# Kernel tuning notes

Measured on AMD Instinct MI355X. Metric: run time of the kernel, lower is better.

The kernel has to match this reference:

```python
import jax, jax.numpy as jnp
import numpy as np

N_GOAL, N_OBS, N_TASK = 16384, 65536, 8192
E1, E2 = 1048576, 1048576
B = 256            # graphs in batch
F, S = 128, 64     # dim_features, dim_state


def setup_inputs() -> dict:
    key = jax.random.key(0)
    ks = jax.random.split(key, 16)
    inp = {
        "x_goal": jax.random.normal(ks[0], (N_GOAL, F), jnp.float32),
        "x_obs": jax.random.normal(ks[1], (N_OBS, F), jnp.float32),
        "x_task": jax.random.normal(ks[2], (N_TASK, S), jnp.float32),
        "ei_go_src": jax.random.randint(ks[3], (E1,), 0, N_GOAL),
        "ei_go_dst": jax.random.randint(ks[4], (E1,), 0, N_OBS),
        "ei_ot_src": jax.random.randint(ks[5], (E2,), 0, N_OBS),
        "ei_ot_dst": jax.random.randint(ks[6], (E2,), 0, N_TASK),
        # contiguous graph assignment: 32 task nodes per graph
        "task_batch": jnp.arange(N_TASK) // (N_TASK // B),
        # GinStandardMLP (state_gin): Lin(F,S)-ReLU-Lin(S,S)-ReLU
        "W1": jax.random.normal(ks[7], (F, S), jnp.float32) * 0.05,
        "b1": jnp.zeros((S,), jnp.float32),
        "W2": jax.random.normal(ks[8], (S, S), jnp.float32) * 0.05,
        "b2": jnp.zeros((S,), jnp.float32),
        # GinUnactivatedMLP (action_gin): Lin(S,S)-ReLU-Lin(S,1)
        "W3": jax.random.normal(ks[9], (S, S), jnp.float32) * 0.05,
        "b3": jnp.zeros((S,), jnp.float32),
        "W4": jax.random.normal(ks[10], (S, 1), jnp.float32) * 0.05,
        "b4": jnp.zeros((1,), jnp.float32),
        # critic head: Lin(2,8)-ReLU-Lin(8,1)
        "Wc1": jax.random.normal(ks[11], (2, 8), jnp.float32) * 0.5,
        "bc1": jnp.zeros((8,), jnp.float32),
        "Wc2": jax.random.normal(ks[12], (8, 1), jnp.float32) * 0.5,
        "bc2": jnp.zeros((1,), jnp.float32),
    }
    return inp


def reference(x_goal, x_obs, x_task,
              ei_go_src, ei_go_dst, ei_ot_src, ei_ot_dst, task_batch,
              W1, b1, W2, b2, W3, b3, W4, b4, Wc1, bc1, Wc2, bc2):
    # --- state_gin: GINConv((goal, obs)), eps=0 ---
    agg1 = jax.ops.segment_sum(x_goal[ei_go_src], ei_go_dst, num_segments=N_OBS)
    h = x_obs + agg1                              # (1+eps)*x_dst + sum_j x_src
    h = jax.nn.relu(h @ W1 + b1)
    x1 = jax.nn.relu(h @ W2 + b2)                 # [N_OBS, S]

    # --- action_gin: GINConv((obs, task)), eps=0 ---
    agg2 = jax.ops.segment_sum(x1[ei_ot_src], ei_ot_dst, num_segments=N_TASK)
    g = x_task + agg2
    g = jax.nn.relu(g @ W3 + b3)
    x2 = g @ W4 + b4                              # [N_TASK, 1]

    # --- critic path: global max / mean pool over task nodes per graph ---
    max_pool = jax.ops.segment_max(x2, task_batch, num_segments=B)   # [B, 1]
    cnt = jax.ops.segment_sum(jnp.ones((N_TASK, 1), x2.dtype), task_batch, num_segments=B)
    mean_pool = jax.ops.segment_sum(x2, task_batch, num_segments=B) / cnt  # [B, 1]

    pooled = jnp.concatenate([max_pool.max(axis=1, keepdims=True),
                              mean_pool.mean(axis=1, keepdims=True)], axis=1)  # [B, 2]
    out = jax.nn.relu(pooled @ Wc1 + bc1) @ Wc2 + bc2                 # [B, 1]
    return out.squeeze(-1)                                            # [B]
```

## Files before the change

### kernel.cpp

```cpp
#include <hip/hip_runtime.h>
#include <hip/hip_bf16.h>


#define CAP1 2816
#define CAP2 5120
#define GEMM_BLKS 640

__global__ __launch_bounds__(256) void prep(
    const float* __restrict__ x_goal, const float* __restrict__ x_obs,
    const float* __restrict__ W, float* __restrict__ xg1,
    float* __restrict__ obs,
    const int* __restrict__ go_src, const int* __restrict__ go_dst,
    const int* __restrict__ ot_src, const int* __restrict__ ot_dst,
    int* __restrict__ gcur1, int* __restrict__ gcur2,
    int* __restrict__ pairs1, int* __restrict__ pairs2, int nblk1, int nblk2,
    const float* __restrict__ W2, const float* __restrict__ W3,
    float* __restrict__ w2t_g, float* __restrict__ w3t_g)
{
    __shared__ float smem[8192];
    const int tid = threadIdx.x;

    if (blockIdx.x < GEMM_BLKS) {
        const float* X;
        float* O;
        int row0;
        if (blockIdx.x < 128) { X = x_goal; O = xg1; row0 = blockIdx.x * 128; }
        else                  { X = x_obs;  O = obs; row0 = (blockIdx.x - 128) * 128; }
        const int c0 = (tid & 7) * 8;
        const int trow = tid >> 3;
        const int r0 = trow * 4;
        const int swz = trow & 7;
        const int w = tid >> 6;
        const int lane = tid & 63;
        const int srow = w * 32 + (lane >> 3);
        const int skbx = lane & 7;

        float acc[4][8];
        #pragma unroll
        for (int i = 0; i < 4; ++i)
            #pragma unroll
            for (int j = 0; j < 8; ++j) acc[i][j] = 0.f;

        float* bufA = smem;
        float* bufB = smem + 4096;

        auto stage = [&](float* buf, int k0) {
            #pragma unroll
            for (int m = 0; m < 4; ++m) {
                int row = srow + m * 8;
                int kg = skbx ^ ((row >> 2) & 7);
                const float* gp = X + (size_t)(row0 + row) * 128 + k0 + kg * 4;
                __builtin_amdgcn_global_load_lds(
                    (const __attribute__((address_space(1))) unsigned int*)gp,
                    (__attribute__((address_space(3))) unsigned int*)
                        (buf + (w * 4 + m) * 256),
                    16, 0, 0);
            }
        };

        stage(bufA, 0);
        __syncthreads();

        float* cur = bufA;
        float* nxt = bufB;
        for (int kc = 0; kc < 4; ++kc) {
            const int k0 = kc * 32;
            if (kc < 3) stage(nxt, k0 + 32);
            #pragma unroll 2
            for (int kb = 0; kb < 8; ++kb) {
                float4 xv[4];
                #pragma unroll
                for (int i = 0; i < 4; ++i)
                    xv[i] = *(const float4*)(cur + (r0 + i) * 32 + ((kb ^ swz) << 2));
                #pragma unroll
                for (int kk = 0; kk < 4; ++kk) {
                    const float* wp = W + (size_t)(k0 + kb * 4 + kk) * 64 + c0;
                    float4 w0 = *(const float4*)(wp);
                    float4 w1 = *(const float4*)(wp + 4);
                    #pragma unroll
                    for (int i = 0; i < 4; ++i) {
                        float xk = (kk == 0) ? xv[i].x : (kk == 1) ? xv[i].y
                                 : (kk == 2) ? xv[i].z : xv[i].w;
                        acc[i][0] = fmaf(xk, w0.x, acc[i][0]);
                        acc[i][1] = fmaf(xk, w0.y, acc[i][1]);
                        acc[i][2] = fmaf(xk, w0.z, acc[i][2]);
                        acc[i][3] = fmaf(xk, w0.w, acc[i][3]);
                        acc[i][4] = fmaf(xk, w1.x, acc[i][4]);
                        acc[i][5] = fmaf(xk, w1.y, acc[i][5]);
                        acc[i][6] = fmaf(xk, w1.z, acc[i][6]);
                        acc[i][7] = fmaf(xk, w1.w, acc[i][7]);
                    }
                }
            }
            __syncthreads();
            float* t = cur; cur = nxt; nxt = t;
        }
        #pragma unroll
        for (int i = 0; i < 4; ++i) {
            float4 o0; o0.x = acc[i][0]; o0.y = acc[i][1]; o0.z = acc[i][2]; o0.w = acc[i][3];
            float4 o1; o1.x = acc[i][4]; o1.y = acc[i][5]; o1.z = acc[i][6]; o1.w = acc[i][7];
            float* p = O + (size_t)(row0 + r0 + i) * 64 + c0;
            *(float4*)p = o0;
            *(float4*)(p + 4) = o1;
        }
    } else if (blockIdx.x < GEMM_BLKS + nblk1 + nblk2) {
        int* hist = (int*)smem;
        int* cur  = (int*)smem + 512;
        const int blk2 = blockIdx.x - GEMM_BLKS;
        const bool s1 = blk2 < nblk1;
        const int* src = s1 ? go_src : ot_src;
        const int* dst = s1 ? go_dst : ot_dst;
        int* gcur  = s1 ? gcur1 : gcur2;
        int* pairs = s1 ? pairs1 : pairs2;
        const int bsh  = s1 ? 7 : 5;
        const int rowm = s1 ? 127 : 31;
        const int nb   = s1 ? 512 : 256;
        const int cap  = s1 ? CAP1 : CAP2;
        const int blk  = s1 ? blk2 : blk2 - nblk1;

        for (int i = tid; i < nb; i += 256) hist[i] = 0;
        __syncthreads();
        const int base = blk * 4096;
        const int4* d4 = (const int4*)(dst + base);
        const int4* s4 = (const int4*)(src + base);
        int4 dv[4];
        #pragma unroll
        for (int k = 0; k < 4; ++k) {
            dv[k] = d4[k * 256 + tid];
            atomicAdd(&hist[dv[k].x >> bsh], 1);
            atomicAdd(&hist[dv[k].y >> bsh], 1);
            atomicAdd(&hist[dv[k].z >> bsh], 1);
            atomicAdd(&hist[dv[k].w >> bsh], 1);
        }
        __syncthreads();
        for (int i = tid; i < nb; i += 256)
            cur[i] = atomicAdd(&gcur[i], hist[i]);
        __syncthreads();
        #pragma unroll
        for (int k = 0; k < 4; ++k) {
            int4 sv = s4[k * 256 + tid];
            int d, s, b, p;
            d = dv[k].x; s = sv.x; b = d >> bsh; p = atomicAdd(&cur[b], 1);
            if (p < cap) pairs[(size_t)b * cap + p] = ((d & rowm) << 17) | s;
            d = dv[k].y; s = sv.y; b = d >> bsh; p = atomicAdd(&cur[b], 1);
            if (p < cap) pairs[(size_t)b * cap + p] = ((d & rowm) << 17) | s;
            d = dv[k].z; s = sv.z; b = d >> bsh; p = atomicAdd(&cur[b], 1);
            if (p < cap) pairs[(size_t)b * cap + p] = ((d & rowm) << 17) | s;
            d = dv[k].w; s = sv.w; b = d >> bsh; p = atomicAdd(&cur[b], 1);
            if (p < cap) pairs[(size_t)b * cap + p] = ((d & rowm) << 17) | s;
        }
    } else {
        for (int i = tid; i < 4352; i += 256) {
            int c = i / 68, k = i % 68;
            float v2 = (k < 64) ? W2[k * 64 + c] : 0.f;
            float v3 = (k < 64) ? W3[k * 64 + c] : 0.f;
            w2t_g[i] = v2;
            w3t_g[i] = v3;
        }
    }
}

__global__ __launch_bounds__(1024) void gather_mlp_obs(
    const int* __restrict__ pairs, const int* __restrict__ cnt,
    const float* __restrict__ xg1, const float* __restrict__ obs,
    const float* __restrict__ b1, const float* __restrict__ w2t_g,
    const float* __restrict__ b2, float* __restrict__ x1)
{
    constexpr int ROWS = 128;
    __shared__ __align__(16) int ssrc[CAP1];
    __shared__ int offs[ROWS + 1];
    __shared__ int rcnt[ROWS];
    __shared__ __align__(16) float W2t[64 * 68];
    __shared__ __align__(16) float hb[16 * 64];
    const int tid = threadIdx.x;
    const int b = blockIdx.x;

    #pragma unroll
    for (int i = tid; i < 4352; i += 1024) W2t[i] = w2t_g[i];
    if (tid < ROWS) rcnt[tid] = 0;
    __syncthreads();
    int n = cnt[b];
    if (n > CAP1) n = CAP1;
    const int* bp = pairs + (size_t)b * CAP1;

    int e0 = -1, e1 = -1, e2 = -1;
    {
        int i = tid;
        if (i < n) {
            e0 = bp[i]; atomicAdd(&rcnt[e0 >> 17], 1); i += 1024;
            if (i < n) {
                e1 = bp[i]; atomicAdd(&rcnt[e1 >> 17], 1); i += 1024;
                if (i < n) { e2 = bp[i]; atomicAdd(&rcnt[e2 >> 17], 1); }
            }
        }
    }
    __syncthreads();
    if (tid < 64) {
        int v0 = rcnt[2 * tid], v1 = rcnt[2 * tid + 1];
        int s = v0 + v1;
        #pragma unroll
        for (int d = 1; d < 64; d <<= 1) {
            int t = __shfl_up(s, d);
            if (tid >= d) s += t;
        }
        int ex = s - v0 - v1;
        offs[2 * tid] = ex;
        offs[2 * tid + 1] = ex + v0;
        rcnt[2 * tid] = ex;
        rcnt[2 * tid + 1] = ex + v0;
        if (tid == 63) offs[ROWS] = s;
    }
    __syncthreads();
    if (e0 >= 0) { int p = atomicAdd(&rcnt[e0 >> 17], 1); ssrc[p] = e0 & 0x1FFFF; }
    if (e1 >= 0) { int p = atomicAdd(&rcnt[e1 >> 17], 1); ssrc[p] = e1 & 0x1FFFF; }
    if (e2 >= 0) { int p = atomicAdd(&rcnt[e2 >> 17], 1); ssrc[p] = e2 & 0x1FFFF; }
    __syncthreads();
    const int wv = tid >> 6;
    const int lane = tid & 63;
    const float bb1 = b1[lane];
    const float bb2 = b2[lane];
    float* hp = hb + wv * 64;
    const float4* h4 = (const float4*)hp;
    const float4* wrow = (const float4*)(W2t + lane * 68);
    for (int r = wv; r < ROWS; r += 16) {
        int beg = offs[r], end = offs[r + 1];
        size_t gi = (((size_t)b * ROWS) + r) * 64 + lane;
        float base = obs[gi];
        float a0 = 0.f, a1 = 0.f, a2 = 0.f, a3 = 0.f;
        float a4 = 0.f, a5 = 0.f, a6 = 0.f, a7 = 0.f;
        int e = beg;
        for (; e < end && (e & 3); ++e)
            a0 += xg1[(size_t)ssrc[e] * 64 + lane];
        for (; e + 8 <= end; e += 8) {
            int4 s0 = *(const int4*)(ssrc + e);
            int4 s1 = *(const int4*)(ssrc + e + 4);
            a0 += xg1[(size_t)s0.x * 64 + lane];
            a1 += xg1[(size_t)s0.y * 64 + lane];
            a2 += xg1[(size_t)s0.z * 64 + lane];
            a3 += xg1[(size_t)s0.w * 64 + lane];
            a4 += xg1[(size_t)s1.x * 64 + lane];
            a5 += xg1[(size_t)s1.y * 64 + lane];
            a6 += xg1[(size_t)s1.z * 64 + lane];
            a7 += xg1[(size_t)s1.w * 64 + lane];
        }
        for (; e + 4 <= end; e += 4) {
            int4 s0 = *(const int4*)(ssrc + e);
            a0 += xg1[(size_t)s0.x * 64 + lane];
            a1 += xg1[(size_t)s0.y * 64 + lane];
            a2 += xg1[(size_t)s0.z * 64 + lane];
            a3 += xg1[(size_t)s0.w * 64 + lane];
        }
        for (; e < end; ++e)
            a0 += xg1[(size_t)ssrc[e] * 64 + lane];
        float acc = ((a0 + a1) + (a2 + a3)) + ((a4 + a5) + (a6 + a7)) + base;
        hp[lane] = fmaxf(acc + bb1, 0.f);
        float a = bb2;
        #pragma unroll 8
        for (int kc = 0; kc < 16; ++kc) {
            float4 hv = h4[kc];
            float4 wv4 = wrow[kc];
            a = fmaf(hv.x, wv4.x, a);
            a = fmaf(hv.y, wv4.y, a);
            a = fmaf(hv.z, wv4.z, a);
            a = fmaf(hv.w, wv4.w, a);
        }
        x1[gi] = fmaxf(a, 0.f);
    }
}

__global__ __launch_bounds__(1024) void gather_mlp_task_pool(
    const int* __restrict__ pairs, const int* __restrict__ cnt,
    const float* __restrict__ x1, const float* __restrict__ x_task,
    const float* __restrict__ w3t_g, const float* __restrict__ b3,
    const float* __restrict__ W4, const float* __restrict__ b4,
    const float* __restrict__ Wc1, const float* __restrict__ bc1,
    const float* __restrict__ Wc2, const float* __restrict__ bc2,
    float* __restrict__ out)
{
    constexpr int ROWS = 32;
    __shared__ __align__(16) int ssrc[CAP2];
    __shared__ int offs[ROWS + 1];
    __shared__ int rcnt[ROWS];
    __shared__ __align__(16) float W3t[64 * 68];
    __shared__ __align__(16) float hb[16 * 64];
    __shared__ float xrow[ROWS];
    const int tid = threadIdx.x;
    const int b = blockIdx.x;

    #pragma unroll
    for (int i = tid; i < 4352; i += 1024) W3t[i] = w3t_g[i];
    if (tid < ROWS) rcnt[tid] = 0;
    __syncthreads();
    int n = cnt[b];
    if (n > CAP2) n = CAP2;
    const int* bp = pairs + (size_t)b * CAP2;

    int e0 = -1, e1 = -1, e2 = -1, e3 = -1, e4 = -1;
    {
        int i = tid;
        if (i < n) { e0 = bp[i]; atomicAdd(&rcnt[e0 >> 17], 1); i += 1024;
        if (i < n) { e1 = bp[i]; atomicAdd(&rcnt[e1 >> 17], 1); i += 1024;
        if (i < n) { e2 = bp[i]; atomicAdd(&rcnt[e2 >> 17], 1); i += 1024;
        if (i < n) { e3 = bp[i]; atomicAdd(&rcnt[e3 >> 17], 1); i += 1024;
        if (i < n) { e4 = bp[i]; atomicAdd(&rcnt[e4 >> 17], 1); } } } } }
    }
    __syncthreads();
    if (tid < 32) {
        int v = rcnt[tid];
        int s = v;
        #pragma unroll
        for (int d = 1; d < 32; d <<= 1) {
            int t = __shfl_up(s, d);
            if (tid >= d) s += t;
        }
        int ex = s - v;
        offs[tid] = ex;
        rcnt[tid] = ex;
        if (tid == 31) offs[ROWS] = s;
    }
    __syncthreads();
    if (e0 >= 0) { int p = atomicAdd(&rcnt[e0 >> 17], 1); ssrc[p] = e0 & 0x1FFFF; }
    if (e1 >= 0) { int p = atomicAdd(&rcnt[e1 >> 17], 1); ssrc[p] = e1 & 0x1FFFF; }
    if (e2 >= 0) { int p = atomicAdd(&rcnt[e2 >> 17], 1); ssrc[p] = e2 & 0x1FFFF; }
    if (e3 >= 0) { int p = atomicAdd(&rcnt[e3 >> 17], 1); ssrc[p] = e3 & 0x1FFFF; }
    if (e4 >= 0) { int p = atomicAdd(&rcnt[e4 >> 17], 1); ssrc[p] = e4 & 0x1FFFF; }
    __syncthreads();

    const int wv = tid >> 6;
    const int lane = tid & 63;
    const float bb3 = b3[lane];
    const float w4l = W4[lane];
    const float b4c = b4[0];
    float* hp = hb + wv * 64;
    const float4* h4 = (const float4*)hp;
    const float4* wrow = (const float4*)(W3t + lane * 68);
    #pragma unroll
    for (int half = 0; half < 2; ++half) {
        const int r = wv + half * 16;
        const int row = b * ROWS + r;
        int beg = offs[r], end = offs[r + 1];
        float base = x_task[(size_t)row * 64 + lane];
        float a0 = 0.f, a1 = 0.f, a2 = 0.f, a3 = 0.f;
        float a4 = 0.f, a5 = 0.f, a6 = 0.f, a7 = 0.f;
        int e = beg;
        for (; e < end && (e & 3); ++e)
            a0 += x1[(size_t)ssrc[e] * 64 + lane];
        for (; e + 8 <= end; e += 8) {
            int4 s0 = *(const int4*)(ssrc + e);
            int4 s1 = *(const int4*)(ssrc + e + 4);
            a0 += x1[(size_t)s0.x * 64 + lane];
            a1 += x1[(size_t)s0.y * 64 + lane];
            a2 += x1[(size_t)s0.z * 64 + lane];
            a3 += x1[(size_t)s0.w * 64 + lane];
            a4 += x1[(size_t)s1.x * 64 + lane];
            a5 += x1[(size_t)s1.y * 64 + lane];
            a6 += x1[(size_t)s1.z * 64 + lane];
            a7 += x1[(size_t)s1.w * 64 + lane];
        }
        for (; e + 4 <= end; e += 4) {
            int4 s0 = *(const int4*)(ssrc + e);
            a0 += x1[(size_t)s0.x * 64 + lane];
            a1 += x1[(size_t)s0.y * 64 + lane];
            a2 += x1[(size_t)s0.z * 64 + lane];
            a3 += x1[(size_t)s0.w * 64 + lane];
        }
        for (; e < end; ++e)
            a0 += x1[(size_t)ssrc[e] * 64 + lane];
        float t = ((a0 + a1) + (a2 + a3)) + ((a4 + a5) + (a6 + a7)) + base;
        hp[lane] = t;
        float a = bb3;
        #pragma unroll 8
        for (int kc = 0; kc < 16; ++kc) {
            float4 hv = h4[kc];
            float4 wv4 = wrow[kc];
            a = fmaf(hv.x, wv4.x, a);
            a = fmaf(hv.y, wv4.y, a);
            a = fmaf(hv.z, wv4.z, a);
            a = fmaf(hv.w, wv4.w, a);
        }
        float p = fmaxf(a, 0.f) * w4l;
        p += __shfl_xor(p, 1);
        p += __shfl_xor(p, 2);
        p += __shfl_xor(p, 4);
        p += __shfl_xor(p, 8);
        p += __shfl_xor(p, 16);
        p += __shfl_xor(p, 32);
        if (lane == 0) xrow[r] = p + b4c;
    }
    __syncthreads();
    if (tid == 0) {
        float mx = -1e30f, sm = 0.f;
        #pragma unroll
        for (int i = 0; i < ROWS; ++i) {
            float v = xrow[i];
            mx = fmaxf(mx, v);
            sm += v;
        }
        float mn = sm * (1.f / 32.f);
        float o = bc2[0];
        #pragma unroll
        for (int j = 0; j < 8; ++j) {
            float t = fmaxf(mx * Wc1[j] + mn * Wc1[8 + j] + bc1[j], 0.f);
            o = fmaf(t, Wc2[j], o);
        }
        out[b] = o;
    }
}

extern "C" void kernel_launch(void* const* d_in, const int* in_sizes, int n_in,
                              void* d_out, int out_size, void* d_ws, size_t ws_size,
                              hipStream_t stream)
{
    const float* x_goal = (const float*)d_in[0];
    const float* x_obs  = (const float*)d_in[1];
    const float* x_task = (const float*)d_in[2];
    const int* go_src = (const int*)d_in[3];
    const int* go_dst = (const int*)d_in[4];
    const int* ot_src = (const int*)d_in[5];
    const int* ot_dst = (const int*)d_in[6];
    const float* W1  = (const float*)d_in[8];
    const float* b1  = (const float*)d_in[9];
    const float* W2  = (const float*)d_in[10];
    const float* b2  = (const float*)d_in[11];
    const float* W3  = (const float*)d_in[12];
    const float* b3  = (const float*)d_in[13];
    const float* W4  = (const float*)d_in[14];
    const float* b4  = (const float*)d_in[15];
    const float* Wc1 = (const float*)d_in[16];
    const float* bc1 = (const float*)d_in[17];
    const float* Wc2 = (const float*)d_in[18];
    const float* bc2 = (const float*)d_in[19];
    float* out = (float*)d_out;

    const int N_OBS = 65536, N_GOAL = 16384;
    const int E1 = in_sizes[3], E2 = in_sizes[5];
    const int NB1 = 512, NB2 = 256;

    char* w = (char*)d_ws;
    float* obs    = (float*)w;  w += (size_t)N_OBS * 64 * 4;
    float* x1     = (float*)w;  w += (size_t)N_OBS * 64 * 4;
    float* xg1    = (float*)w;  w += (size_t)N_GOAL * 64 * 4;
    int*   pairs1 = (int*)w;    w += (size_t)NB1 * CAP1 * 4;
    int*   pairs2 = (int*)w;    w += (size_t)NB2 * CAP2 * 4;
    int*   gcur1  = (int*)w;    w += NB1 * 4;
    int*   gcur2  = (int*)w;    w += NB2 * 4;
    float* w2t_g  = (float*)w;  w += 64 * 68 * 4;
    float* w3t_g  = (float*)w;  w += 64 * 68 * 4;

    hipMemsetAsync(gcur1, 0, (NB1 + NB2) * 4, stream);

    const int nblk1 = E1 / 4096;
    const int nblk2 = E2 / 4096;
    prep<<<GEMM_BLKS + nblk1 + nblk2 + 1, 256, 0, stream>>>(
        x_goal, x_obs, W1, xg1, obs,
        go_src, go_dst, ot_src, ot_dst, gcur1, gcur2, pairs1, pairs2,
        nblk1, nblk2, W2, W3, w2t_g, w3t_g);
    gather_mlp_obs<<<NB1, 1024, 0, stream>>>(pairs1, gcur1, xg1, obs, b1, w2t_g, b2, x1);
    gather_mlp_task_pool<<<NB2, 1024, 0, stream>>>(pairs2, gcur2, x1, x_task,
                                                   w3t_g, b3, W4, b4,
                                                   Wc1, bc1, Wc2, bc2, out);
}
```

Measured before the change: 230.7 us.

## Fuse obs and task gather kernels with a global completion counter

Merges the two gather+MLP kernels into one launch. The first 512 blocks handle obs rows and increment a device-scope done counter. The remaining 256 blocks build their task-edge CSR in shared memory first, then spin until all obs blocks finish before gathering x1. This is meant to remove a kernel launch boundary and overlap the task-side edge bucketing with the obs phase. It risks deadlock if the spinning blocks take up CUs before the obs blocks are scheduled; that relies on in-order block dispatch. Spinning also wastes occupancy.

```diff
diff --git a/kernel.cpp b/kernel.cpp
--- a/kernel.cpp
+++ b/kernel.cpp
@@ -5,6 +5,8 @@
 #define CAP1 2816
 #define CAP2 5120
 #define GEMM_BLKS 640
+#define NB1 512
+#define NB2 256
 
 __global__ __launch_bounds__(256) void prep(
     const float* __restrict__ x_goal, const float* __restrict__ x_obs,
@@ -160,250 +162,262 @@
     }
 }
 
-__global__ __launch_bounds__(1024) void gather_mlp_obs(
-    const int* __restrict__ pairs, const int* __restrict__ cnt,
+__global__ __launch_bounds__(1024) void gather_fused(
+    const int* __restrict__ pairs1, const int* __restrict__ gcur1,
+    const int* __restrict__ pairs2, const int* __restrict__ gcur2,
     const float* __restrict__ xg1, const float* __restrict__ obs,
     const float* __restrict__ b1, const float* __restrict__ w2t_g,
-    const float* __restrict__ b2, float* __restrict__ x1)
-{
-    constexpr int ROWS = 128;
-    __shared__ __align__(16) int ssrc[CAP1];
-    __shared__ int offs[ROWS + 1];
-    __shared__ int rcnt[ROWS];
-    __shared__ __align__(16) float W2t[64 * 68];
-    __shared__ __align__(16) float hb[16 * 64];
-    const int tid = threadIdx.x;
-    const int b = blockIdx.x;
-
-    #pragma unroll
-    for (int i = tid; i < 4352; i += 1024) W2t[i] = w2t_g[i];
-    if (tid < ROWS) rcnt[tid] = 0;
-    __syncthreads();
-    int n = cnt[b];
-    if (n > CAP1) n = CAP1;
-    const int* bp = pairs + (size_t)b * CAP1;
-
-    int e0 = -1, e1 = -1, e2 = -1;
-    {
-        int i = tid;
-        if (i < n) {
-            e0 = bp[i]; atomicAdd(&rcnt[e0 >> 17], 1); i += 1024;
-            if (i < n) {
-                e1 = bp[i]; atomicAdd(&rcnt[e1 >> 17], 1); i += 1024;
-                if (i < n) { e2 = bp[i]; atomicAdd(&rcnt[e2 >> 17], 1); }
-            }
-        }
-    }
-    __syncthreads();
-    if (tid < 64) {
-        int v0 = rcnt[2 * tid], v1 = rcnt[2 * tid + 1];
-        int s = v0 + v1;
-        #pragma unroll
-        for (int d = 1; d < 64; d <<= 1) {
-            int t = __shfl_up(s, d);
-            if (tid >= d) s += t;
-        }
-        int ex = s - v0 - v1;
-        offs[2 * tid] = ex;
-        offs[2 * tid + 1] = ex + v0;
-        rcnt[2 * tid] = ex;
-        rcnt[2 * tid + 1] = ex + v0;
-        if (tid == 63) offs[ROWS] = s;
-    }
-    __syncthreads();
-    if (e0 >= 0) { int p = atomicAdd(&rcnt[e0 >> 17], 1); ssrc[p] = e0 & 0x1FFFF; }
-    if (e1 >= 0) { int p = atomicAdd(&rcnt[e1 >> 17], 1); ssrc[p] = e1 & 0x1FFFF; }
-    if (e2 >= 0) { int p = atomicAdd(&rcnt[e2 >> 17], 1); ssrc[p] = e2 & 0x1FFFF; }
-    __syncthreads();
-    const int wv = tid >> 6;
-    const int lane = tid & 63;
-    const float bb1 = b1[lane];
-    const float bb2 = b2[lane];
-    float* hp = hb + wv * 64;
-    const float4* h4 = (const float4*)hp;
-    const float4* wrow = (const float4*)(W2t + lane * 68);
-    for (int r = wv; r < ROWS; r += 16) {
-        int beg = offs[r], end = offs[r + 1];
-        size_t gi = (((size_t)b * ROWS) + r) * 64 + lane;
-        float base = obs[gi];
-        float a0 = 0.f, a1 = 0.f, a2 = 0.f, a3 = 0.f;
-        float a4 = 0.f, a5 = 0.f, a6 = 0.f, a7 = 0.f;
-        int e = beg;
-        for (; e < end && (e & 3); ++e)
-            a0 += xg1[(size_t)ssrc[e] * 64 + lane];
-        for (; e + 8 <= end; e += 8) {
-            int4 s0 = *(const int4*)(ssrc + e);
-            int4 s1 = *(const int4*)(ssrc + e + 4);
-            a0 += xg1[(size_t)s0.x * 64 + lane];
-            a1 += xg1[(size_t)s0.y * 64 + lane];
-            a2 += xg1[(size_t)s0.z * 64 + lane];
-            a3 += xg1[(size_t)s0.w * 64 + lane];
-            a4 += xg1[(size_t)s1.x * 64 + lane];
-            a5 += xg1[(size_t)s1.y * 64 + lane];
-            a6 += xg1[(size_t)s1.z * 64 + lane];
-            a7 += xg1[(size_t)s1.w * 64 + lane];
-        }
-        for (; e + 4 <= end; e += 4) {
-            int4 s0 = *(const int4*)(ssrc + e);
-            a0 += xg1[(size_t)s0.x * 64 + lane];
-            a1 += xg1[(size_t)s0.y * 64 + lane];
-            a2 += xg1[(size_t)s0.z * 64 + lane];
-            a3 += xg1[(size_t)s0.w * 64 + lane];
-        }
-        for (; e < end; ++e)
-            a0 += xg1[(size_t)ssrc[e] * 64 + lane];
-        float acc = ((a0 + a1) + (a2 + a3)) + ((a4 + a5) + (a6 + a7)) + base;
-        hp[lane] = fmaxf(acc + bb1, 0.f);
-        float a = bb2;
-        #pragma unroll 8
-        for (int kc = 0; kc < 16; ++kc) {
-            float4 hv = h4[kc];
-            float4 wv4 = wrow[kc];
-            a = fmaf(hv.x, wv4.x, a);
-            a = fmaf(hv.y, wv4.y, a);
-            a = fmaf(hv.z, wv4.z, a);
-            a = fmaf(hv.w, wv4.w, a);
-        }
-        x1[gi] = fmaxf(a, 0.f);
-    }
-}
-
-__global__ __launch_bounds__(1024) void gather_mlp_task_pool(
-    const int* __restrict__ pairs, const int* __restrict__ cnt,
-    const float* __restrict__ x1, const float* __restrict__ x_task,
+    const float* __restrict__ b2, float* __restrict__ x1,
+    const float* __restrict__ x_task,
     const float* __restrict__ w3t_g, const float* __restrict__ b3,
     const float* __restrict__ W4, const float* __restrict__ b4,
     const float* __restrict__ Wc1, const float* __restrict__ bc1,
     const float* __restrict__ Wc2, const float* __restrict__ bc2,
-    float* __restrict__ out)
+    float* __restrict__ out, int* __restrict__ done)
 {
-    constexpr int ROWS = 32;
-    __shared__ __align__(16) int ssrc[CAP2];
-    __shared__ int offs[ROWS + 1];
-    __shared__ int rcnt[ROWS];
-    __shared__ __align__(16) float W3t[64 * 68];
-    __shared__ __align__(16) float hb[16 * 64];
-    __shared__ float xrow[ROWS];
+    __shared__ __align__(16) char sm[42376];
     const int tid = threadIdx.x;
-    const int b = blockIdx.x;
-
-    #pragma unroll
-    for (int i = tid; i < 4352; i += 1024) W3t[i] = w3t_g[i];
-    if (tid < ROWS) rcnt[tid] = 0;
-    __syncthreads();
-    int n = cnt[b];
-    if (n > CAP2) n = CAP2;
-    const int* bp = pairs + (size_t)b * CAP2;
-
-    int e0 = -1, e1 = -1, e2 = -1, e3 = -1, e4 = -1;
-    {
-        int i = tid;
-        if (i < n) { e0 = bp[i]; atomicAdd(&rcnt[e0 >> 17], 1); i += 1024;
-        if (i < n) { e1 = bp[i]; atomicAdd(&rcnt[e1 >> 17], 1); i += 1024;
-        if (i < n) { e2 = bp[i]; atomicAdd(&rcnt[e2 >> 17], 1); i += 1024;
-        if (i < n) { e3 = bp[i]; atomicAdd(&rcnt[e3 >> 17], 1); i += 1024;
-        if (i < n) { e4 = bp[i]; atomicAdd(&rcnt[e4 >> 17], 1); } } } } }
-    }
-    __syncthreads();
-    if (tid < 32) {
-        int v = rcnt[tid];
-        int s = v;
-        #pragma unroll
-        for (int d = 1; d < 32; d <<= 1) {
-            int t = __shfl_up(s, d);
-            if (tid >= d) s += t;
-        }
-        int ex = s - v;
-        offs[tid] = ex;
-        rcnt[tid] = ex;
-        if (tid == 31) offs[ROWS] = s;
-    }
-    __syncthreads();
-    if (e0 >= 0) { int p = atomicAdd(&rcnt[e0 >> 17], 1); ssrc[p] = e0 & 0x1FFFF; }
-    if (e1 >= 0) { int p = atomicAdd(&rcnt[e1 >> 17], 1); ssrc[p] = e1 & 0x1FFFF; }
-    if (e2 >= 0) { int p = atomicAdd(&rcnt[e2 >> 17], 1); ssrc[p] = e2 & 0x1FFFF; }
-    if (e3 >= 0) { int p = atomicAdd(&rcnt[e3 >> 17], 1); ssrc[p] = e3 & 0x1FFFF; }
-    if (e4 >= 0) { int p = atomicAdd(&rcnt[e4 >> 17], 1); ssrc[p] = e4 & 0x1FFFF; }
-    __syncthreads();
-
-    const int wv = tid >> 6;
-    const int lane = tid & 63;
-    const float bb3 = b3[lane];
-    const float w4l = W4[lane];
-    const float b4c = b4[0];
-    float* hp = hb + wv * 64;
-    const float4* h4 = (const float4*)hp;
-    const float4* wrow = (const float4*)(W3t + lane * 68);
-    #pragma unroll
-    for (int half = 0; half < 2; ++half) {
-        const int r = wv + half * 16;
-        const int row = b * ROWS + r;
-        int beg = offs[r], end = offs[r + 1];
-        float base = x_task[(size_t)row * 64 + lane];
-        float a0 = 0.f, a1 = 0.f, a2 = 0.f, a3 = 0.f;
-        float a4 = 0.f, a5 = 0.f, a6 = 0.f, a7 = 0.f;
-        int e = beg;
-        for (; e < end && (e & 3); ++e)
-            a0 += x1[(size_t)ssrc[e] * 64 + lane];
-        for (; e + 8 <= end; e += 8) {
-            int4 s0 = *(const int4*)(ssrc + e);
-            int4 s1 = *(const int4*)(ssrc + e + 4);
-            a0 += x1[(size_t)s0.x * 64 + lane];
-            a1 += x1[(size_t)s0.y * 64 + lane];
-            a2 += x1[(size_t)s0.z * 64 + lane];
-            a3 += x1[(size_t)s0.w * 64 + lane];
-            a4 += x1[(size_t)s1.x * 64 + lane];
-            a5 += x1[(size_t)s1.y * 64 + lane];
-            a6 += x1[(size_t)s1.z * 64 + lane];
-            a7 += x1[(size_t)s1.w * 64 + lane];
-        }
-        for (; e + 4 <= end; e += 4) {
-            int4 s0 = *(const int4*)(ssrc + e);
-            a0 += x1[(size_t)s0.x * 64 + lane];
-            a1 += x1[(size_t)s0.y * 64 + lane];
-            a2 += x1[(size_t)s0.z * 64 + lane];
-            a3 += x1[(size_t)s0.w * 64 + lane];
-        }
-        for (; e < end; ++e)
-            a0 += x1[(size_t)ssrc[e] * 64 + lane];
-        float t = ((a0 + a1) + (a2 + a3)) + ((a4 + a5) + (a6 + a7)) + base;
-        hp[lane] = t;
-        float a = bb3;
-        #pragma unroll 8
-        for (int kc = 0; kc < 16; ++kc) {
-            float4 hv = h4[kc];
-            float4 wv4 = wrow[kc];
-            a = fmaf(hv.x, wv4.x, a);
-            a = fmaf(hv.y, wv4.y, a);
-            a = fmaf(hv.z, wv4.z, a);
-            a = fmaf(hv.w, wv4.w, a);
-        }
-        float p = fmaxf(a, 0.f) * w4l;
-        p += __shfl_xor(p, 1);
-        p += __shfl_xor(p, 2);
-        p += __shfl_xor(p, 4);
-        p += __shfl_xor(p, 8);
-        p += __shfl_xor(p, 16);
-        p += __shfl_xor(p, 32);
-        if (lane == 0) xrow[r] = p + b4c;
-    }
-    __syncthreads();
-    if (tid == 0) {
-        float mx = -1e30f, sm = 0.f;
-        #pragma unroll
-        for (int i = 0; i < ROWS; ++i) {
-            float v = xrow[i];
-            mx = fmaxf(mx, v);
-            sm += v;
-        }
-        float mn = sm * (1.f / 32.f);
-        float o = bc2[0];
-        #pragma unroll
-        for (int j = 0; j < 8; ++j) {
-            float t = fmaxf(mx * Wc1[j] + mn * Wc1[8 + j] + bc1[j], 0.f);
-            o = fmaf(t, Wc2[j], o);
-        }
-        out[b] = o;
+
+    if (blockIdx.x < NB1) {
+        constexpr int ROWS = 128;
+        float* W2t = (float*)(sm);
+        float* hb  = (float*)(sm + 17408);
+        int* ssrc  = (int*)(sm + 21504);
+        int* offs  = (int*)(sm + 32768);
+        int* rcnt  = (int*)(sm + 33284);
+        const int b = blockIdx.x;
+
+        #pragma unroll
+        for (int i = tid; i < 4352; i += 1024) W2t[i] = w2t_g[i];
+        if (tid < ROWS) rcnt[tid] = 0;
+        __syncthreads();
+        int n = gcur1[b];
+        if (n > CAP1) n = CAP1;
+        const int* bp = pairs1 + (size_t)b * CAP1;
+
+        int e0 = -1, e1 = -1, e2 = -1;
+        {
+            int i = tid;
+            if (i < n) {
+                e0 = bp[i]; atomicAdd(&rcnt[e0 >> 17], 1); i += 1024;
+                if (i < n) {
+                    e1 = bp[i]; atomicAdd(&rcnt[e1 >> 17], 1); i += 1024;
+                    if (i < n) { e2 = bp[i]; atomicAdd(&rcnt[e2 >> 17], 1); }
+                }
+            }
+        }
+        __syncthreads();
+        if (tid < 64) {
+            int v0 = rcnt[2 * tid], v1 = rcnt[2 * tid + 1];
+            int s = v0 + v1;
+            #pragma unroll
+            for (int d = 1; d < 64; d <<= 1) {
+                int t = __shfl_up(s, d);
+                if (tid >= d) s += t;
+            }
+            int ex = s - v0 - v1;
+            offs[2 * tid] = ex;
+            offs[2 * tid + 1] = ex + v0;
+            rcnt[2 * tid] = ex;
+            rcnt[2 * tid + 1] = ex + v0;
+            if (tid == 63) offs[ROWS] = s;
+        }
+        __syncthreads();
+        if (e0 >= 0) { int p = atomicAdd(&rcnt[e0 >> 17], 1); ssrc[p] = e0 & 0x1FFFF; }
+        if (e1 >= 0) { int p = atomicAdd(&rcnt[e1 >> 17], 1); ssrc[p] = e1 & 0x1FFFF; }
+        if (e2 >= 0) { int p = atomicAdd(&rcnt[e2 >> 17], 1); ssrc[p] = e2 & 0x1FFFF; }
+        __syncthreads();
+        const int wv = tid >> 6;
+        const int lane = tid & 63;
+        const float bb1 = b1[lane];
+        const float bb2 = b2[lane];
+        float* hp = hb + wv * 64;
+        const float4* h4 = (const float4*)hp;
+        const float4* wrow = (const float4*)(W2t + lane * 68);
+        for (int r = wv; r < ROWS; r += 16) {
+            int beg = offs[r], end = offs[r + 1];
+            size_t gi = (((size_t)b * ROWS) + r) * 64 + lane;
+            float base = obs[gi];
+            float a0 = 0.f, a1 = 0.f, a2 = 0.f, a3 = 0.f;
+            float a4 = 0.f, a5 = 0.f, a6 = 0.f, a7 = 0.f;
+            int e = beg;
+            for (; e < end && (e & 3); ++e)
+                a0 += xg1[(size_t)ssrc[e] * 64 + lane];
+            for (; e + 8 <= end; e += 8) {
+                int4 s0 = *(const int4*)(ssrc + e);
+                int4 s1 = *(const int4*)(ssrc + e + 4);
+                a0 += xg1[(size_t)s0.x * 64 + lane];
+                a1 += xg1[(size_t)s0.y * 64 + lane];
+                a2 += xg1[(size_t)s0.z * 64 + lane];
+                a3 += xg1[(size_t)s0.w * 64 + lane];
+                a4 += xg1[(size_t)s1.x * 64 + lane];
+                a5 += xg1[(size_t)s1.y * 64 + lane];
+                a6 += xg1[(size_t)s1.z * 64 + lane];
+                a7 += xg1[(size_t)s1.w * 64 + lane];
+            }
+            for (; e + 4 <= end; e += 4) {
+                int4 s0 = *(const int4*)(ssrc + e);
+                a0 += xg1[(size_t)s0.x * 64 + lane];
+                a1 += xg1[(size_t)s0.y * 64 + lane];
+                a2 += xg1[(size_t)s0.z * 64 + lane];
+                a3 += xg1[(size_t)s0.w * 64 + lane];
+            }
+            for (; e < end; ++e)
+                a0 += xg1[(size_t)ssrc[e] * 64 + lane];
+            float acc = ((a0 + a1) + (a2 + a3)) + ((a4 + a5) + (a6 + a7)) + base;
+            hp[lane] = fmaxf(acc + bb1, 0.f);
+            float a = bb2;
+            #pragma unroll 8
+            for (int kc = 0; kc < 16; ++kc) {
+                float4 hv = h4[kc];
+                float4 wv4 = wrow[kc];
+                a = fmaf(hv.x, wv4.x, a);
+                a = fmaf(hv.y, wv4.y, a);
+                a = fmaf(hv.z, wv4.z, a);
+                a = fmaf(hv.w, wv4.w, a);
+            }
+            x1[gi] = fmaxf(a, 0.f);
+        }
+        __syncthreads();
+        if (tid == 0) {
+            __threadfence();
+            __hip_atomic_fetch_add(done, 1, __ATOMIC_RELEASE,
+                                   __HIP_MEMORY_SCOPE_AGENT);
+        }
+    } else {
+        constexpr int ROWS = 32;
+        float* W3t  = (float*)(sm);
+        float* hb   = (float*)(sm + 17408);
+        int* ssrc   = (int*)(sm + 21504);
+        int* offs   = (int*)(sm + 41984);
+        int* rcnt   = (int*)(sm + 42116);
+        float* xrow = (float*)(sm + 42244);
+        const int b = blockIdx.x - NB1;
+
+        #pragma unroll
+        for (int i = tid; i < 4352; i += 1024) W3t[i] = w3t_g[i];
+        if (tid < ROWS) rcnt[tid] = 0;
+        __syncthreads();
+        int n = gcur2[b];
+        if (n > CAP2) n = CAP2;
+        const int* bp = pairs2 + (size_t)b * CAP2;
+
+        int e0 = -1, e1 = -1, e2 = -1, e3 = -1, e4 = -1;
+        {
+            int i = tid;
+            if (i < n) { e0 = bp[i]; atomicAdd(&rcnt[e0 >> 17], 1); i += 1024;
+            if (i < n) { e1 = bp[i]; atomicAdd(&rcnt[e1 >> 17], 1); i += 1024;
+            if (i < n) { e2 = bp[i]; atomicAdd(&rcnt[e2 >> 17], 1); i += 1024;
+            if (i < n) { e3 = bp[i]; atomicAdd(&rcnt[e3 >> 17], 1); i += 1024;
+            if (i < n) { e4 = bp[i]; atomicAdd(&rcnt[e4 >> 17], 1); } } } } }
+        }
+        __syncthreads();
+        if (tid < 32) {
+            int v = rcnt[tid];
+            int s = v;
+            #pragma unroll
+            for (int d = 1; d < 32; d <<= 1) {
+                int t = __shfl_up(s, d);
+                if (tid >= d) s += t;
+            }
+            int ex = s - v;
+            offs[tid] = ex;
+            rcnt[tid] = ex;
+            if (tid == 31) offs[ROWS] = s;
+        }
+        __syncthreads();
+        if (e0 >= 0) { int p = atomicAdd(&rcnt[e0 >> 17], 1); ssrc[p] = e0 & 0x1FFFF; }
+        if (e1 >= 0) { int p = atomicAdd(&rcnt[e1 >> 17], 1); ssrc[p] = e1 & 0x1FFFF; }
+        if (e2 >= 0) { int p = atomicAdd(&rcnt[e2 >> 17], 1); ssrc[p] = e2 & 0x1FFFF; }
+        if (e3 >= 0) { int p = atomicAdd(&rcnt[e3 >> 17], 1); ssrc[p] = e3 & 0x1FFFF; }
+        if (e4 >= 0) { int p = atomicAdd(&rcnt[e4 >> 17], 1); ssrc[p] = e4 & 0x1FFFF; }
+        __syncthreads();
+
+        if (tid == 0) {
+            while (__hip_atomic_load(done, __ATOMIC_ACQUIRE,
+                                     __HIP_MEMORY_SCOPE_AGENT) < NB1) {}
+        }
+        __syncthreads();
+
+        const int wv = tid >> 6;
+        const int lane = tid & 63;
+        const float bb3 = b3[lane];
+        const float w4l = W4[lane];
+        const float b4c = b4[0];
+        float* hp = hb + wv * 64;
+        const float4* h4 = (const float4*)hp;
+        const float4* wrow = (const float4*)(W3t + lane * 68);
+        #pragma unroll
+        for (int half = 0; half < 2; ++half) {
+            const int r = wv + half * 16;
+            const int row = b * ROWS + r;
+            int beg = offs[r], end = offs[r + 1];
+            float base = x_task[(size_t)row * 64 + lane];
+            float a0 = 0.f, a1 = 0.f, a2 = 0.f, a3 = 0.f;
+            float a4 = 0.f, a5 = 0.f, a6 = 0.f, a7 = 0.f;
+            int e = beg;
+            for (; e < end && (e & 3); ++e)
+                a0 += x1[(size_t)ssrc[e] * 64 + lane];
+            for (; e + 8 <= end; e += 8) {
+                int4 s0 = *(const int4*)(ssrc + e);
+                int4 s1 = *(const int4*)(ssrc + e + 4);
+                a0 += x1[(size_t)s0.x * 64 + lane];
+                a1 += x1[(size_t)s0.y * 64 + lane];
+                a2 += x1[(size_t)s0.z * 64 + lane];
+                a3 += x1[(size_t)s0.w * 64 + lane];
+                a4 += x1[(size_t)s1.x * 64 + lane];
+                a5 += x1[(size_t)s1.y * 64 + lane];
+                a6 += x1[(size_t)s1.z * 64 + lane];
+                a7 += x1[(size_t)s1.w * 64 + lane];
+            }
+            for (; e + 4 <= end; e += 4) {
+                int4 s0 = *(const int4*)(ssrc + e);
+                a0 += x1[(size_t)s0.x * 64 + lane];
+                a1 += x1[(size_t)s0.y * 64 + lane];
+                a2 += x1[(size_t)s0.z * 64 + lane];
+                a3 += x1[(size_t)s0.w * 64 + lane];
+            }
+            for (; e < end; ++e)
+                a0 += x1[(size_t)ssrc[e] * 64 + lane];
+            float t = ((a0 + a1) + (a2 + a3)) + ((a4 + a5) + (a6 + a7)) + base;
+            hp[lane] = t;
+            float a = bb3;
+            #pragma unroll 8
+            for (int kc = 0; kc < 16; ++kc) {
+                float4 hv = h4[kc];
+                float4 wv4 = wrow[kc];
+                a = fmaf(hv.x, wv4.x, a);
+                a = fmaf(hv.y, wv4.y, a);
+                a = fmaf(hv.z, wv4.z, a);
+                a = fmaf(hv.w, wv4.w, a);
+            }
+            float p = fmaxf(a, 0.f) * w4l;
+            p += __shfl_xor(p, 1);
+            p += __shfl_xor(p, 2);
+            p += __shfl_xor(p, 4);
+            p += __shfl_xor(p, 8);
+            p += __shfl_xor(p, 16);
+            p += __shfl_xor(p, 32);
+            if (lane == 0) xrow[r] = p + b4c;
+        }
+        __syncthreads();
+        if (tid == 0) {
+            float mx = -1e30f, sm2 = 0.f;
+            #pragma unroll
+            for (int i = 0; i < ROWS; ++i) {
+                float v = xrow[i];
+                mx = fmaxf(mx, v);
+                sm2 += v;
+            }
+            float mn = sm2 * (1.f / 32.f);
+            float o = bc2[0];
+            #pragma unroll
+            for (int j = 0; j < 8; ++j) {
+                float t = fmaxf(mx * Wc1[j] + mn * Wc1[8 + j] + bc1[j], 0.f);
+                o = fmaf(t, Wc2[j], o);
+            }
+            out[b] = o;
+        }
     }
 }
 
@@ -434,7 +448,6 @@
 
     const int N_OBS = 65536, N_GOAL = 16384;
     const int E1 = in_sizes[3], E2 = in_sizes[5];
-    const int NB1 = 512, NB2 = 256;
 
     char* w = (char*)d_ws;
     float* obs    = (float*)w;  w += (size_t)N_OBS * 64 * 4;
@@ -444,10 +457,11 @@
     int*   pairs2 = (int*)w;    w += (size_t)NB2 * CAP2 * 4;
     int*   gcur1  = (int*)w;    w += NB1 * 4;
     int*   gcur2  = (int*)w;    w += NB2 * 4;
+    int*   done   = (int*)w;    w += 4;
     float* w2t_g  = (float*)w;  w += 64 * 68 * 4;
     float* w3t_g  = (float*)w;  w += 64 * 68 * 4;
 
-    hipMemsetAsync(gcur1, 0, (NB1 + NB2) * 4, stream);
+    hipMemsetAsync(gcur1, 0, (NB1 + NB2 + 1) * 4, stream);
 
     const int nblk1 = E1 / 4096;
     const int nblk2 = E2 / 4096;
@@ -455,8 +469,7 @@
         x_goal, x_obs, W1, xg1, obs,
         go_src, go_dst, ot_src, ot_dst, gcur1, gcur2, pairs1, pairs2,
         nblk1, nblk2, W2, W3, w2t_g, w3t_g);
-    gather_mlp_obs<<<NB1, 1024, 0, stream>>>(pairs1, gcur1, xg1, obs, b1, w2t_g, b2, x1);
-    gather_mlp_task_pool<<<NB2, 1024, 0, stream>>>(pairs2, gcur2, x1, x_task,
-                                                   w3t_g, b3, W4, b4,
-                                                   Wc1, bc1, Wc2, bc2, out);
+    gather_fused<<<NB1 + NB2, 1024, 0, stream>>>(
+        pairs1, gcur1, pairs2, gcur2, xg1, obs, b1, w2t_g, b2, x1,
+        x_task, w3t_g, b3, W4, b4, Wc1, bc1, Wc2, bc2, out, done);
 }
```

Result: slower. 275.1 us (+19.3%).
